# Performance work log

Measured on AMD Instinct MI355X. Metric: run time of the kernel, lower is better.

Reference implementation:

```python
import jax, jax.numpy as jnp
import numpy as np

B, K, I, H, O = 256, 512, 64, 512, 1


def setup_inputs() -> dict:
    key = jax.random.key(0)
    ks = jax.random.split(key, 4)
    return {
        "input_seq": jax.random.normal(ks[0], (B, K, I), dtype=jnp.float32),
        "kernel": jax.random.normal(ks[1], (I, 4 * H), dtype=jnp.float32) * (2.0 / I) ** 0.5,
        "recurrent_kernel": jax.random.normal(ks[2], (4 * H, H), dtype=jnp.float32) * (2.0 / H) ** 0.5,
        "bias": jnp.zeros((4 * H,), dtype=jnp.float32),
        "Woutput": jax.random.normal(ks[3], (O, H), dtype=jnp.float32) * (2.0 / H) ** 0.5,
        "boutput": jnp.zeros((O,), dtype=jnp.float32),
    }


def reference(input_seq, kernel, recurrent_kernel, bias, Woutput, boutput):
    Bsz, Kt, _ = input_seq.shape
    Hs = recurrent_kernel.shape[1]
    # Precompute input projections for all timesteps: (K, B, 4H)
    x_proj = jnp.einsum("bki,ig->kbg", input_seq, kernel)

    def step(carry, x_t):
        h, c = carry
        # F.linear(h, recurrent_kernel, bias) == h @ recurrent_kernel.T + bias
        gates = x_t + h @ recurrent_kernel.T + bias  # (B, 4H)
        f_g, i_g, c_g, o_g = jnp.split(gates, 4, axis=1)
        f = jax.nn.sigmoid(f_g)
        i = jax.nn.sigmoid(i_g)
        c_prime = jnp.tanh(c_g)
        c_t = f * c + i * c_prime
        o = jax.nn.sigmoid(o_g)
        h_t = o * jnp.tanh(c_t)
        return (h_t, c_t), None

    h0 = jnp.zeros((Bsz, Hs), dtype=input_seq.dtype)
    c0 = jnp.zeros((Bsz, Hs), dtype=input_seq.dtype)
    (h_last, _), _ = jax.lax.scan(step, (h0, c0), x_proj)
    # Output layer applied to last timestep only (only lstm_out of final step is used)
    out = h_last @ Woutput.T + boutput  # (B, O)
    return out.reshape(-1)
```

## Files before the change

### kernel.cpp

```cpp
#include <hip/hip_runtime.h>

#define TSTEPS 512
#define BATCH  256
#define ISZ    64
#define HSZ    512
#define GSZ    2048
#define NKT    18
#define BG     16
#define PLANE64 65536

typedef __attribute__((ext_vector_type(8))) short short8;
typedef __attribute__((ext_vector_type(4))) float f32x4;
typedef __attribute__((ext_vector_type(4))) unsigned int u32x4;
typedef unsigned long long u64t;

static __device__ __forceinline__ unsigned short f2bf(float f) {
    unsigned int u = __float_as_uint(f);
    return (unsigned short)((u + 0x7fffu + ((u >> 16) & 1u)) >> 16);
}
static __device__ __forceinline__ float sig_(float x) {
    return 1.0f / (1.0f + __expf(-x));
}
static __device__ __forceinline__ float tanh_(float x) {
    float e = __expf(-2.0f * fabsf(x));
    float t = (1.0f - e) / (1.0f + e);
    return copysignf(t, x);
}
static __device__ __forceinline__ u64t ld_tag64(const u64t* p) {
    return __hip_atomic_load(p, __ATOMIC_RELAXED, __HIP_MEMORY_SCOPE_AGENT);
}
static __device__ __forceinline__ void st_tag64(u64t* p, u64t v) {
    __hip_atomic_store(p, v, __ATOMIC_RELAXED, __HIP_MEMORY_SCOPE_AGENT);
}

__global__ void pack_w(const float* __restrict__ R, const float* __restrict__ Kin,
                       unsigned short* __restrict__ wpack)
{
    const int t  = blockIdx.x * 256 + threadIdx.x;
    const int l  = t & 63;
    const int kt = (t >> 6) % NKT;
    const int m  = (t / (64 * NKT)) & 7;
    const int jj = t / (64 * NKT * 8);
    const int r   = 16 * m + (l & 15);
    const int q   = r & 3;
    const int hco = r >> 2;
    const int grow  = q * HSZ + jj * 32 + hco;
    const int kbase = kt * 32 + (l >> 4) * 8;
    unsigned int pk[4];
#pragma unroll
    for (int p = 0; p < 4; ++p) {
        const int k0 = kbase + 2 * p;
        const int k1 = k0 + 1;
        const float f0 = (k0 < HSZ) ? R[(size_t)grow * HSZ + k0]
                                    : Kin[(size_t)(k0 - HSZ) * GSZ + grow];
        const float f1 = (k1 < HSZ) ? R[(size_t)grow * HSZ + k1]
                                    : Kin[(size_t)(k1 - HSZ) * GSZ + grow];
        pk[p] = (unsigned)f2bf(f0) | ((unsigned)f2bf(f1) << 16);
    }
    uint4 v = make_uint4(pk[0], pk[1], pk[2], pk[3]);
    *reinterpret_cast<uint4*>(wpack + (size_t)t * 8) = v;
}

__global__ void zero_tags(u32x4* __restrict__ hb) {
    u32x4 z = {0u, 0u, 0u, 0u};
    hb[blockIdx.x * 256 + threadIdx.x] = z;
}

__global__ __launch_bounds__(256, 1) void lstm_persist(
    const unsigned short* __restrict__ wpack,
    const float* __restrict__ input_seq,
    const float* __restrict__ bias,
    unsigned int* __restrict__ tbuf,
    float* __restrict__ hlast)
{
    __shared__ __align__(16) unsigned short lds_B[16][584];
    __shared__ __align__(16) unsigned short lds_hn[16][40];
    const int tid = threadIdx.x;
    const int bid = blockIdx.x;
    const int gi = bid & 15;
    const int jw = bid >> 4;
    const int jj = jw;

    const int w  = tid >> 6;
    const int l  = tid & 63;
    const int bb = l & 15;
    const int lg = l >> 4;
    const int m0 = 2 * w, m1 = 2 * w + 1;

    short8 wA[NKT], wB[NKT];
#pragma unroll
    for (int kt = 0; kt < NKT; ++kt) {
        wA[kt] = *reinterpret_cast<const short8*>(
            wpack + (((size_t)(jj * 8 + m0) * NKT + kt) * 64 + l) * 8);
        wB[kt] = *reinterpret_cast<const short8*>(
            wpack + (((size_t)(jj * 8 + m1) * NKT + kt) * 64 + l) * 8);
    }
#pragma unroll
    for (int kt = 0; kt < NKT; ++kt) {
        asm volatile("" : "+a"(wA[kt]));
        asm volatile("" : "+a"(wB[kt]));
    }
    const int hc0 = 4 * m0 + lg, hc1 = 4 * m1 + lg;
    const int gh0 = jj * 32 + hc0, gh1 = jj * 32 + hc1;
    float bs0[4], bs1[4];
#pragma unroll
    for (int qg = 0; qg < 4; ++qg) {
        bs0[qg] = bias[qg * HSZ + gh0];
        bs1[qg] = bias[qg * HSZ + gh1];
    }

    float c0 = 0.f, c1 = 0.f;

    const int sb = tid & 15, sc = tid >> 4;
    const float* xbase = input_seq + (size_t)(gi * BG + sb) * (TSTEPS * ISZ) + sc * 4;
    float4 xr = *reinterpret_cast<const float4*>(xbase);

    const u64t* const hb0 = reinterpret_cast<const u64t*>(tbuf);
    const u64t* const hb1 = reinterpret_cast<const u64t*>(tbuf) + PLANE64;
    const int rr = tid >> 4, cch = tid & 15;
    const size_t csrc = (size_t)(gi * BG + rr) * 256 + cch;
    const int b_ = tid >> 4, pr = tid & 15;
    const size_t pdst = ((size_t)(gi * BG + b_) * HSZ + jw * 32 + pr * 2) >> 1;

    for (int s = 0; s < TSTEPS; ++s) {
        {
            uint2 px;
            px.x = (unsigned)f2bf(xr.x) | ((unsigned)f2bf(xr.y) << 16);
            px.y = (unsigned)f2bf(xr.z) | ((unsigned)f2bf(xr.w) << 16);
            *reinterpret_cast<uint2*>(&lds_B[sb][HSZ + sc * 4]) = px;
            if (s + 1 < TSTEPS)
                xr = *reinterpret_cast<const float4*>(xbase + (size_t)(s + 1) * ISZ);
        }
        if (s > 0) {
            const u64t* src = ((s & 1) ? hb1 : hb0) + csrc;
            const u64t want = ((u64t)(unsigned)s << 48) | ((u64t)(unsigned)s << 16);
            u64t v[16];
            bool ok;
            do {
                ok = true;
#pragma unroll
                for (int i = 0; i < 16; ++i)
                    v[i] = ld_tag64(src + (size_t)i * 16);
#pragma unroll
                for (int i = 0; i < 16; ++i)
                    ok = ok && ((v[i] & 0xFFFF0000FFFF0000ull) == want);
            } while (!ok);
#pragma unroll
            for (int i = 0; i < 16; ++i) {
                const unsigned d = (unsigned)(v[i] & 0xFFFFu) |
                                   ((unsigned)(v[i] >> 16) & 0xFFFF0000u);
                *reinterpret_cast<unsigned*>(&lds_B[rr][i * 32 + cch * 2]) = d;
            }
        } else {
#pragma unroll
            for (int i = 0; i < 16; ++i)
                *reinterpret_cast<unsigned*>(&lds_B[rr][i * 32 + cch * 2]) = 0u;
        }
        __syncthreads();

        f32x4 acc0 = {bs0[0], bs0[1], bs0[2], bs0[3]};
        f32x4 acc1 = {bs1[0], bs1[1], bs1[2], bs1[3]};
#pragma unroll
        for (int kt = 0; kt < NKT; ++kt) {
            const short8 bf = *reinterpret_cast<const short8*>(
                &lds_B[bb][kt * 32 + lg * 8]);
            acc0 = __builtin_amdgcn_mfma_f32_16x16x32_bf16(wA[kt], bf, acc0, 0, 0, 0);
            acc1 = __builtin_amdgcn_mfma_f32_16x16x32_bf16(wB[kt], bf, acc1, 0, 0, 0);
        }

        const float fg0 = sig_(acc0[0]);
        const float ig0 = sig_(acc0[1]);
        const float cp0 = tanh_(acc0[2]);
        const float og0 = sig_(acc0[3]);
        c0 = fg0 * c0 + ig0 * cp0;
        const float h0v = og0 * tanh_(c0);
        const float fg1 = sig_(acc1[0]);
        const float ig1 = sig_(acc1[1]);
        const float cp1 = tanh_(acc1[2]);
        const float og1 = sig_(acc1[3]);
        c1 = fg1 * c1 + ig1 * cp1;
        const float h1v = og1 * tanh_(c1);

        if (s == TSTEPS - 1) {
            hlast[(size_t)(gi * BG + bb) * HSZ + gh0] = h0v;
            hlast[(size_t)(gi * BG + bb) * HSZ + gh1] = h1v;
            break;
        }
        lds_hn[bb][hc0] = f2bf(h0v);
        lds_hn[bb][hc1] = f2bf(h1v);
        __syncthreads();

        {
            const unsigned h2 = *reinterpret_cast<const unsigned*>(&lds_hn[b_][pr * 2]);
            const unsigned t16 = (unsigned)(s + 1) << 16;
            const unsigned lo = (h2 & 0xFFFFu) | t16;
            const unsigned hi = (h2 >> 16) | t16;
            const u64t tagged = ((u64t)hi << 32) | (u64t)lo;
            u64t* dst = (u64t*)(tbuf) + (size_t)((s + 1) & 1) * PLANE64 + pdst;
            st_tag64(dst, tagged);
        }
    }
}

__global__ void out_kernel(const float* __restrict__ hlast,
                           const float* __restrict__ wout,
                           const float* __restrict__ bout,
                           float* __restrict__ out)
{
    const int b = blockIdx.x;
    const int l = threadIdx.x;
    float p = 0.f;
    for (int k = l; k < HSZ; k += 64)
        p += hlast[(size_t)b * HSZ + k] * wout[k];
    for (int off = 32; off > 0; off >>= 1)
        p += __shfl_down(p, off, 64);
    if (l == 0) out[b] = p + bout[0];
}

extern "C" void kernel_launch(void* const* d_in, const int* in_sizes, int n_in,
                              void* d_out, int out_size, void* d_ws, size_t ws_size,
                              hipStream_t stream) {
    const float* input_seq = (const float*)d_in[0];
    const float* Kin       = (const float*)d_in[1];
    const float* R         = (const float*)d_in[2];
    const float* bias      = (const float*)d_in[3];
    const float* Wout      = (const float*)d_in[4];
    const float* bout      = (const float*)d_in[5];
    float* out = (float*)d_out;

    char* ws = (char*)d_ws;
    unsigned short* wpack = (unsigned short*)(ws);
    unsigned int* tbuf    = (unsigned int*)(ws + 2359296);
    float* hlast          = (float*)(ws + 2359296 + 1048576);

    zero_tags<<<dim3(256), dim3(256), 0, stream>>>((u32x4*)tbuf);
    pack_w<<<dim3(576), dim3(256), 0, stream>>>(R, Kin, wpack);
    lstm_persist<<<dim3(256), dim3(256), 0, stream>>>(
        wpack, input_seq, bias, tbuf, hlast);
    out_kernel<<<dim3(256), dim3(64), 0, stream>>>(hlast, Wout, bout, out);
}
```

Measured before the change: 1.129 ms.

## Split hidden columns finer and interleave two batch groups per block

Each block now owns 16 hidden columns (instead of 32) and processes two batch groups (p and p+8) alternately within each timestep, using separate LDS buffers for each. Each wave now holds one weight fragment set instead of two, halving register-resident weights. While one group's matmul and gate math run, the other group's h exchange from other blocks can complete, hiding cross-block synchronization latency. The cost is an extra __syncthreads pair per half and more tagged-store traffic per block.

```diff
diff --git a/kernel.cpp b/kernel.cpp
--- a/kernel.cpp
+++ b/kernel.cpp
@@ -39,23 +39,23 @@
     const int t  = blockIdx.x * 256 + threadIdx.x;
     const int l  = t & 63;
     const int kt = (t >> 6) % NKT;
-    const int m  = (t / (64 * NKT)) & 7;
-    const int jj = t / (64 * NKT * 8);
+    const int m  = (t / (64 * NKT)) & 3;
+    const int jp = t / (64 * NKT * 4);
     const int r   = 16 * m + (l & 15);
     const int q   = r & 3;
     const int hco = r >> 2;
-    const int grow  = q * HSZ + jj * 32 + hco;
+    const int grow  = q * HSZ + jp * 16 + hco;
     const int kbase = kt * 32 + (l >> 4) * 8;
     unsigned int pk[4];
 #pragma unroll
-    for (int p = 0; p < 4; ++p) {
-        const int k0 = kbase + 2 * p;
+    for (int pp = 0; pp < 4; ++pp) {
+        const int k0 = kbase + 2 * pp;
         const int k1 = k0 + 1;
         const float f0 = (k0 < HSZ) ? R[(size_t)grow * HSZ + k0]
                                     : Kin[(size_t)(k0 - HSZ) * GSZ + grow];
         const float f1 = (k1 < HSZ) ? R[(size_t)grow * HSZ + k1]
                                     : Kin[(size_t)(k1 - HSZ) * GSZ + grow];
-        pk[p] = (unsigned)f2bf(f0) | ((unsigned)f2bf(f1) << 16);
+        pk[pp] = (unsigned)f2bf(f0) | ((unsigned)f2bf(f1) << 16);
     }
     uint4 v = make_uint4(pk[0], pk[1], pk[2], pk[3]);
     *reinterpret_cast<uint4*>(wpack + (size_t)t * 8) = v;
@@ -73,133 +73,129 @@
     unsigned int* __restrict__ tbuf,
     float* __restrict__ hlast)
 {
-    __shared__ __align__(16) unsigned short lds_B[16][584];
-    __shared__ __align__(16) unsigned short lds_hn[16][40];
+    __shared__ __align__(16) unsigned short ldsA[16][584];
+    __shared__ __align__(16) unsigned short ldsB2[16][584];
+    __shared__ __align__(16) unsigned short hnA[16][16];
+    __shared__ __align__(16) unsigned short hnB[16][16];
     const int tid = threadIdx.x;
     const int bid = blockIdx.x;
-    const int gi = bid & 15;
-    const int jw = bid >> 4;
-    const int jj = jw;
+    const int p   = bid & 7;
+    const int jp  = bid >> 3;
+    const int gA  = p, gB = p + 8;
 
     const int w  = tid >> 6;
     const int l  = tid & 63;
     const int bb = l & 15;
     const int lg = l >> 4;
-    const int m0 = 2 * w, m1 = 2 * w + 1;
-
-    short8 wA[NKT], wB[NKT];
-#pragma unroll
-    for (int kt = 0; kt < NKT; ++kt) {
-        wA[kt] = *reinterpret_cast<const short8*>(
-            wpack + (((size_t)(jj * 8 + m0) * NKT + kt) * 64 + l) * 8);
-        wB[kt] = *reinterpret_cast<const short8*>(
-            wpack + (((size_t)(jj * 8 + m1) * NKT + kt) * 64 + l) * 8);
-    }
-#pragma unroll
-    for (int kt = 0; kt < NKT; ++kt) {
-        asm volatile("" : "+a"(wA[kt]));
-        asm volatile("" : "+a"(wB[kt]));
-    }
-    const int hc0 = 4 * m0 + lg, hc1 = 4 * m1 + lg;
-    const int gh0 = jj * 32 + hc0, gh1 = jj * 32 + hc1;
-    float bs0[4], bs1[4];
-#pragma unroll
-    for (int qg = 0; qg < 4; ++qg) {
-        bs0[qg] = bias[qg * HSZ + gh0];
-        bs1[qg] = bias[qg * HSZ + gh1];
-    }
-
-    float c0 = 0.f, c1 = 0.f;
+
+    short8 wf[NKT];
+#pragma unroll
+    for (int kt = 0; kt < NKT; ++kt)
+        wf[kt] = *reinterpret_cast<const short8*>(
+            wpack + (((size_t)(jp * 4 + w) * NKT + kt) * 64 + l) * 8);
+#pragma unroll
+    for (int kt = 0; kt < NKT; ++kt)
+        asm volatile("" : "+a"(wf[kt]));
+
+    const int hc  = 4 * w + lg;
+    const int ghc = jp * 16 + hc;
+    float bs[4];
+#pragma unroll
+    for (int qg = 0; qg < 4; ++qg) bs[qg] = bias[qg * HSZ + ghc];
+
+    float cA = 0.f, cB = 0.f;
 
     const int sb = tid & 15, sc = tid >> 4;
-    const float* xbase = input_seq + (size_t)(gi * BG + sb) * (TSTEPS * ISZ) + sc * 4;
-    float4 xr = *reinterpret_cast<const float4*>(xbase);
+    const float* xbA = input_seq + (size_t)(gA * BG + sb) * (TSTEPS * ISZ) + sc * 4;
+    const float* xbB = input_seq + (size_t)(gB * BG + sb) * (TSTEPS * ISZ) + sc * 4;
+    float4 xrA = *reinterpret_cast<const float4*>(xbA);
+    float4 xrB = *reinterpret_cast<const float4*>(xbB);
 
     const u64t* const hb0 = reinterpret_cast<const u64t*>(tbuf);
     const u64t* const hb1 = reinterpret_cast<const u64t*>(tbuf) + PLANE64;
     const int rr = tid >> 4, cch = tid & 15;
-    const size_t csrc = (size_t)(gi * BG + rr) * 256 + cch;
-    const int b_ = tid >> 4, pr = tid & 15;
-    const size_t pdst = ((size_t)(gi * BG + b_) * HSZ + jw * 32 + pr * 2) >> 1;
+    const size_t csA = (size_t)(gA * BG + rr) * 256 + cch;
+    const size_t csB = (size_t)(gB * BG + rr) * 256 + cch;
+    const int b_ = tid >> 3, pr = tid & 7;
+    const size_t pdA = (size_t)(gA * BG + b_) * 256 + jp * 8 + pr;
+    const size_t pdB = (size_t)(gB * BG + b_) * 256 + jp * 8 + pr;
+
+    {
+        const int zb = tid >> 4, zc = (tid & 15) * 32;
+        u32x4 z = {0u, 0u, 0u, 0u};
+#pragma unroll
+        for (int i = 0; i < 4; ++i) {
+            reinterpret_cast<u32x4*>(&ldsA[zb][zc])[i]  = z;
+            reinterpret_cast<u32x4*>(&ldsB2[zb][zc])[i] = z;
+        }
+    }
+
+#define DO_HALF(LDSB, HN, XR, XB, CS, PD, CC, G)                                  \
+    {                                                                             \
+                                                 \
+        uint2 px;                                                                 \
+        px.x = (unsigned)f2bf(XR.x) | ((unsigned)f2bf(XR.y) << 16);               \
+        px.y = (unsigned)f2bf(XR.z) | ((unsigned)f2bf(XR.w) << 16);               \
+        *reinterpret_cast<uint2*>(&LDSB[sb][HSZ + sc * 4]) = px;                  \
+        if (s + 1 < TSTEPS)                                                       \
+            XR = *reinterpret_cast<const float4*>(XB + (size_t)(s + 1) * ISZ);    \
+        if (s > 0) {                                                              \
+            const u64t* src = ((s & 1) ? hb1 : hb0) + (CS);                       \
+            const u64t want = ((u64t)(unsigned)s << 48) | ((u64t)(unsigned)s << 16); \
+            u64t v[16];                                                           \
+            bool ok;                                                              \
+            do {                                                                  \
+                ok = true;                                                        \
+                _Pragma("unroll")                                                 \
+                for (int i = 0; i < 16; ++i) v[i] = ld_tag64(src + (size_t)i * 16); \
+                _Pragma("unroll")                                                 \
+                for (int i = 0; i < 16; ++i)                                      \
+                    ok = ok && ((v[i] & 0xFFFF0000FFFF0000ull) == want);          \
+            } while (!ok);                                                        \
+            _Pragma("unroll")                                                     \
+            for (int i = 0; i < 16; ++i) {                                        \
+                const unsigned d = (unsigned)(v[i] & 0xFFFFu) |                   \
+                                   ((unsigned)(v[i] >> 16) & 0xFFFF0000u);        \
+                *reinterpret_cast<unsigned*>(&LDSB[rr][i * 32 + cch * 2]) = d;    \
+            }                                                                     \
+        }                                                                         \
+        __syncthreads();                                    \
+        f32x4 acc = {bs[0], bs[1], bs[2], bs[3]};                                 \
+        _Pragma("unroll")                                                         \
+        for (int kt = 0; kt < NKT; ++kt) {                                        \
+            const short8 bf = *reinterpret_cast<const short8*>(                   \
+                &LDSB[bb][kt * 32 + lg * 8]);                                     \
+            acc = __builtin_amdgcn_mfma_f32_16x16x32_bf16(wf[kt], bf, acc, 0, 0, 0); \
+        }                                                                         \
+        const float fg = sig_(acc[0]);                                            \
+        const float ig = sig_(acc[1]);                                            \
+        const float cp = tanh_(acc[2]);                                           \
+        const float og = sig_(acc[3]);                                            \
+        CC = fg * CC + ig * cp;                                                   \
+        const float hv = og * tanh_(CC);                                          \
+        if (s == TSTEPS - 1) {                                                    \
+            hlast[(size_t)((G) * BG + bb) * HSZ + ghc] = hv;                      \
+        } else {                                                                  \
+            HN[bb][hc] = f2bf(hv);                                                \
+            __syncthreads();                   \
+            if (tid < 128) {                                                      \
+                const unsigned h2 =                                               \
+                    *reinterpret_cast<const unsigned*>(&HN[b_][pr * 2]);          \
+                const unsigned t16 = (unsigned)(s + 1) << 16;                     \
+                const unsigned lo = (h2 & 0xFFFFu) | t16;                         \
+                const unsigned hi = (h2 >> 16) | t16;                             \
+                const u64t tagged = ((u64t)hi << 32) | (u64t)lo;                  \
+                u64t* dst = (u64t*)(tbuf) + (size_t)((s + 1) & 1) * PLANE64 + (PD); \
+                st_tag64(dst, tagged);                                            \
+            }                                                                     \
+        }                                                                         \
+    }
 
     for (int s = 0; s < TSTEPS; ++s) {
-        {
-            uint2 px;
-            px.x = (unsigned)f2bf(xr.x) | ((unsigned)f2bf(xr.y) << 16);
-            px.y = (unsigned)f2bf(xr.z) | ((unsigned)f2bf(xr.w) << 16);
-            *reinterpret_cast<uint2*>(&lds_B[sb][HSZ + sc * 4]) = px;
-            if (s + 1 < TSTEPS)
-                xr = *reinterpret_cast<const float4*>(xbase + (size_t)(s + 1) * ISZ);
-        }
-        if (s > 0) {
-            const u64t* src = ((s & 1) ? hb1 : hb0) + csrc;
-            const u64t want = ((u64t)(unsigned)s << 48) | ((u64t)(unsigned)s << 16);
-            u64t v[16];
-            bool ok;
-            do {
-                ok = true;
-#pragma unroll
-                for (int i = 0; i < 16; ++i)
-                    v[i] = ld_tag64(src + (size_t)i * 16);
-#pragma unroll
-                for (int i = 0; i < 16; ++i)
-                    ok = ok && ((v[i] & 0xFFFF0000FFFF0000ull) == want);
-            } while (!ok);
-#pragma unroll
-            for (int i = 0; i < 16; ++i) {
-                const unsigned d = (unsigned)(v[i] & 0xFFFFu) |
-                                   ((unsigned)(v[i] >> 16) & 0xFFFF0000u);
-                *reinterpret_cast<unsigned*>(&lds_B[rr][i * 32 + cch * 2]) = d;
-            }
-        } else {
-#pragma unroll
-            for (int i = 0; i < 16; ++i)
-                *reinterpret_cast<unsigned*>(&lds_B[rr][i * 32 + cch * 2]) = 0u;
-        }
-        __syncthreads();
-
-        f32x4 acc0 = {bs0[0], bs0[1], bs0[2], bs0[3]};
-        f32x4 acc1 = {bs1[0], bs1[1], bs1[2], bs1[3]};
-#pragma unroll
-        for (int kt = 0; kt < NKT; ++kt) {
-            const short8 bf = *reinterpret_cast<const short8*>(
-                &lds_B[bb][kt * 32 + lg * 8]);
-            acc0 = __builtin_amdgcn_mfma_f32_16x16x32_bf16(wA[kt], bf, acc0, 0, 0, 0);
-            acc1 = __builtin_amdgcn_mfma_f32_16x16x32_bf16(wB[kt], bf, acc1, 0, 0, 0);
-        }
-
-        const float fg0 = sig_(acc0[0]);
-        const float ig0 = sig_(acc0[1]);
-        const float cp0 = tanh_(acc0[2]);
-        const float og0 = sig_(acc0[3]);
-        c0 = fg0 * c0 + ig0 * cp0;
-        const float h0v = og0 * tanh_(c0);
-        const float fg1 = sig_(acc1[0]);
-        const float ig1 = sig_(acc1[1]);
-        const float cp1 = tanh_(acc1[2]);
-        const float og1 = sig_(acc1[3]);
-        c1 = fg1 * c1 + ig1 * cp1;
-        const float h1v = og1 * tanh_(c1);
-
-        if (s == TSTEPS - 1) {
-            hlast[(size_t)(gi * BG + bb) * HSZ + gh0] = h0v;
-            hlast[(size_t)(gi * BG + bb) * HSZ + gh1] = h1v;
-            break;
-        }
-        lds_hn[bb][hc0] = f2bf(h0v);
-        lds_hn[bb][hc1] = f2bf(h1v);
-        __syncthreads();
-
-        {
-            const unsigned h2 = *reinterpret_cast<const unsigned*>(&lds_hn[b_][pr * 2]);
-            const unsigned t16 = (unsigned)(s + 1) << 16;
-            const unsigned lo = (h2 & 0xFFFFu) | t16;
-            const unsigned hi = (h2 >> 16) | t16;
-            const u64t tagged = ((u64t)hi << 32) | (u64t)lo;
-            u64t* dst = (u64t*)(tbuf) + (size_t)((s + 1) & 1) * PLANE64 + pdst;
-            st_tag64(dst, tagged);
-        }
-    }
+        DO_HALF(ldsA,  hnA, xrA, xbA, csA, pdA, cA, gA)
+        DO_HALF(ldsB2, hnB, xrB, xbB, csB, pdB, cB, gB)
+    }
+#undef DO_HALF
 }
 
 __global__ void out_kernel(const float* __restrict__ hlast,
```

New measurement: 1.750 ms. 1.55x slower.
